# Performance work log

Measured on AMD Instinct MI355X. Metric: run time of the kernel, lower is better.

## Reference

```python
import jax, jax.numpy as jnp
import numpy as np

B, S, DIN, DOUT = 2, 2048, 4096, 11008

def setup_inputs() -> dict:
    key = jax.random.key(0)
    k1, k2, k3 = jax.random.split(key, 3)
    x = jax.random.normal(k1, (B, S, DIN), dtype=jnp.float32)
    # int8-range quantized weight codes (stored as int32 for the harness)
    w_int8 = jax.random.randint(k2, (DOUT, DIN), -127, 128, dtype=jnp.int32)
    scale = jnp.float32(0.01)
    bias = jax.random.normal(k3, (DOUT,), dtype=jnp.float32)
    return {"x": x, "w_int8": w_int8, "scale": scale, "bias": bias}

def reference(x, w_int8, scale, bias):
    # Dequantize: weight = int8_codes.astype(float32) * scale  -> [DOUT, DIN]
    weight = w_int8.astype(jnp.float32) * scale
    # F.linear: out = x @ weight.T + bias  -> [B, S, DOUT]
    out = jnp.einsum('bsi,oi->bso', x, weight) + bias
    return out
```

## Files before the change

kernel.cpp:

```cpp
#include <hip/hip_runtime.h>
#include <hip/hip_bf16.h>
#include <stdint.h>

typedef unsigned short u16;

#define M_TOT 4096
#define N_TOT 11008
#define K_TOT 4096

typedef __attribute__((ext_vector_type(4))) int i32x4;
typedef __attribute__((ext_vector_type(4))) float f32x4;
typedef __attribute__((ext_vector_type(8))) short bf16x8;

typedef const __attribute__((address_space(1))) void* gptr_t;
typedef __attribute__((address_space(3))) void* lptr_t;


__global__ __launch_bounds__(256) void quant_x(const float* __restrict__ X,
                                               uint32_t* __restrict__ Xq,
                                               float* __restrict__ scales) {
  int row = blockIdx.x;
  int t = threadIdx.x;
  const float4* xr = reinterpret_cast<const float4*>(X + (size_t)row * K_TOT) + t * 4;
  float4 v[4];
  float m = 0.f;
#pragma unroll
  for (int i = 0; i < 4; ++i) {
    v[i] = xr[i];
    m = fmaxf(m, fmaxf(fmaxf(fabsf(v[i].x), fabsf(v[i].y)),
                       fmaxf(fabsf(v[i].z), fabsf(v[i].w))));
  }
#pragma unroll
  for (int o = 1; o < 64; o <<= 1) m = fmaxf(m, __shfl_xor(m, o));
  __shared__ float wmax[4];
  int w = t >> 6, lane = t & 63;
  if (lane == 0) wmax[w] = m;
  __syncthreads();
  m = fmaxf(fmaxf(wmax[0], wmax[1]), fmaxf(wmax[2], wmax[3]));
  m = fmaxf(m, 1e-30f);
  float inv = 127.f / m;
  uint32_t q[4];
#pragma unroll
  for (int i = 0; i < 4; ++i) {
    int a = (int)rintf(v[i].x * inv), b = (int)rintf(v[i].y * inv);
    int c = (int)rintf(v[i].z * inv), d = (int)rintf(v[i].w * inv);
    q[i] = (a & 0xff) | ((b & 0xff) << 8) | ((c & 0xff) << 16) | ((uint32_t)(d & 0xff) << 24);
  }
  reinterpret_cast<uint4*>(Xq)[(size_t)row * 256 + t] = make_uint4(q[0], q[1], q[2], q[3]);
  if (t == 0) scales[row] = m / 127.f;
}

__global__ __launch_bounds__(256) void cvt_w_q(const int* __restrict__ W,
                                               uint32_t* __restrict__ Wq, int n4) {
  int i = blockIdx.x * 256 + threadIdx.x;
  int stride = gridDim.x * 256;
  for (; i < n4; i += stride) {
    int4 v = reinterpret_cast<const int4*>(W)[i];
    Wq[i] = (v.x & 0xff) | ((v.y & 0xff) << 8) | ((v.z & 0xff) << 16) |
            ((uint32_t)(v.w & 0xff) << 24);
  }
}


#define BM2 256
#define BN2 256
#define BKI 64
#define MT2 (M_TOT / BM2)
#define NT2 (N_TOT / BN2)
#define NWG2 (MT2 * NT2)
#define NKTI (K_TOT / BKI)

__global__ __launch_bounds__(512, 2) void gemm_i8_256(const int8_t* __restrict__ Xq,
                                                      const int8_t* __restrict__ Wq,
                                                      const float* __restrict__ rowsc,
                                                      const float* __restrict__ scale,
                                                      const float* __restrict__ bias,
                                                      float* __restrict__ Out) {
  __shared__ __align__(16) uint8_t lds[4][32768];

  int bid = blockIdx.x;
  int swz = (bid & 7) * (NWG2 / 8) + (bid >> 3);
  int mt = swz & (MT2 - 1);
  int nt = swz >> 4;
  int row0 = mt * BM2, col0 = nt * BN2;

  int t = threadIdx.x;
  int lane = t & 63, w = t >> 6;
  int wm = w >> 2, wn = w & 3;
  int lr = lane & 15, lk = lane >> 4;

  int ci = lane & 3;
  int rA = w * 16 + (lane >> 2);
  int cswz = ci ^ ((rA >> 1) & 3);
  size_t g0 = (size_t)(row0 + rA) * K_TOT + (size_t)(cswz * 16);
  size_t g1 = (size_t)(row0 + 128 + rA) * K_TOT + (size_t)(cswz * 16);
  size_t g2 = (size_t)(col0 + rA) * K_TOT + (size_t)(cswz * 16);
  size_t g3 = (size_t)(col0 + 128 + rA) * K_TOT + (size_t)(cswz * 16);

  auto stageA = [&](int kt) {
    size_t ko = (size_t)kt * BKI;
    char* lb = (char*)(&lds[kt & 3][0]) + w * 1024;
    __builtin_amdgcn_global_load_lds((gptr_t)(const void*)(Xq + g0 + ko), (lptr_t)(void*)(lb), 16, 0, 0);
    __builtin_amdgcn_global_load_lds((gptr_t)(const void*)(Xq + g1 + ko), (lptr_t)(void*)(lb + 8192), 16, 0, 0);
  };
  auto stageB = [&](int kt) {
    size_t ko = (size_t)kt * BKI;
    char* lb = (char*)(&lds[kt & 3][0]) + w * 1024;
    __builtin_amdgcn_global_load_lds((gptr_t)(const void*)(Wq + g2 + ko), (lptr_t)(void*)(lb + 16384), 16, 0, 0);
    __builtin_amdgcn_global_load_lds((gptr_t)(const void*)(Wq + g3 + ko), (lptr_t)(void*)(lb + 24576), 16, 0, 0);
  };

  int aoff[8], boff[4];
#pragma unroll
  for (int m = 0; m < 8; ++m) {
    int ar = wm * 128 + m * 16 + lr;
    aoff[m] = ar * BKI + ((lk ^ ((ar >> 1) & 3)) << 4);
  }
#pragma unroll
  for (int n = 0; n < 4; ++n) {
    int br = wn * 64 + n * 16 + lr;
    boff[n] = 16384 + br * BKI + ((lk ^ ((br >> 1) & 3)) << 4);
  }

  i32x4 acc[8][4] = {};

  auto compute_tile = [&](int kt) {
    const uint8_t* sb = &lds[kt & 3][0];
    i32x4 af[8], bfv[4];
#pragma unroll
    for (int m = 0; m < 8; ++m)
      af[m] = *reinterpret_cast<const i32x4*>(sb + aoff[m]);
#pragma unroll
    for (int n = 0; n < 4; ++n)
      bfv[n] = *reinterpret_cast<const i32x4*>(sb + boff[n]);
    __builtin_amdgcn_s_setprio(1);
#pragma unroll
    for (int m = 0; m < 8; ++m)
#pragma unroll
      for (int n = 0; n < 4; ++n)
        acc[m][n] = __builtin_amdgcn_mfma_i32_16x16x64_i8(af[m], bfv[n], acc[m][n], 0, 0, 0);
    __builtin_amdgcn_s_setprio(0);
  };

  stageA(0); stageB(0);
  stageA(1); stageB(1);
  stageA(2); stageB(2);
  asm volatile("s_waitcnt vmcnt(8)" ::: "memory");
  __builtin_amdgcn_s_barrier();
  asm volatile("" ::: "memory");

#pragma unroll 4
  for (int kt = 0; kt < NKTI - 3; ++kt) {
    const uint8_t* sb = &lds[kt & 3][0];
    i32x4 af[4], af2[4], bfv[4];

#pragma unroll
    for (int m = 0; m < 4; ++m)
      af[m] = *reinterpret_cast<const i32x4*>(sb + aoff[m]);
#pragma unroll
    for (int n = 0; n < 4; ++n)
      bfv[n] = *reinterpret_cast<const i32x4*>(sb + boff[n]);
#pragma unroll
    for (int m = 0; m < 4; ++m)
      af2[m] = *reinterpret_cast<const i32x4*>(sb + aoff[m + 4]);
    stageA(kt + 3);
    __builtin_amdgcn_s_barrier();
    __builtin_amdgcn_s_setprio(1);
#pragma unroll
    for (int m = 0; m < 4; ++m)
#pragma unroll
      for (int n = 0; n < 4; ++n)
        acc[m][n] = __builtin_amdgcn_mfma_i32_16x16x64_i8(af[m], bfv[n], acc[m][n], 0, 0, 0);
    __builtin_amdgcn_s_setprio(0);
    __builtin_amdgcn_s_barrier();
    asm volatile("" ::: "memory");

    stageB(kt + 3);
    asm volatile("s_waitcnt vmcnt(8)" ::: "memory");
    __builtin_amdgcn_s_barrier();
    __builtin_amdgcn_s_setprio(1);
#pragma unroll
    for (int m = 0; m < 4; ++m)
#pragma unroll
      for (int n = 0; n < 4; ++n)
        acc[m + 4][n] = __builtin_amdgcn_mfma_i32_16x16x64_i8(af2[m], bfv[n], acc[m + 4][n], 0, 0, 0);
    __builtin_amdgcn_s_setprio(0);
    __builtin_amdgcn_s_barrier();
    asm volatile("" ::: "memory");
  }

  compute_tile(NKTI - 3);
  asm volatile("s_waitcnt vmcnt(4)" ::: "memory");
  __builtin_amdgcn_s_barrier();
  asm volatile("" ::: "memory");
  compute_tile(NKTI - 2);
  asm volatile("s_waitcnt vmcnt(0)" ::: "memory");
  __builtin_amdgcn_s_barrier();
  asm volatile("" ::: "memory");
  compute_tile(NKTI - 1);

  float scl = scale[0];
  float bv[4];
#pragma unroll
  for (int n = 0; n < 4; ++n)
    bv[n] = bias[col0 + wn * 64 + n * 16 + lr];
#pragma unroll
  for (int m = 0; m < 8; ++m) {
    int rb = row0 + wm * 128 + m * 16 + lk * 4;
    f32x4 srv = *reinterpret_cast<const f32x4*>(rowsc + rb);
#pragma unroll
    for (int n = 0; n < 4; ++n) {
      int col = col0 + wn * 64 + n * 16 + lr;
#pragma unroll
      for (int r = 0; r < 4; ++r)
        Out[(size_t)(rb + r) * N_TOT + col] = (float)acc[m][n][r] * (srv[r] * scl) + bv[n];
    }
  }
}


#define BM 128
#define BN 128
#define BK 32
#define MT (M_TOT / BM)
#define NT (N_TOT / BN)
#define NWG (MT * NT)
#define NK (K_TOT / BK)

__device__ __forceinline__ unsigned pk2_rne(float lo, float hi) {
  unsigned a = __builtin_bit_cast(unsigned, lo);
  unsigned b = __builtin_bit_cast(unsigned, hi);
  a += 0x7FFFu + ((a >> 16) & 1u);
  b += 0x7FFFu + ((b >> 16) & 1u);
  return (a >> 16) | (b & 0xFFFF0000u);
}

__device__ __forceinline__ void mfma_step(const u16* sa, const u16* sb,
                                          f32x4 acc[4][4], int arow, int brow, int lk) {
  bf16x8 af[4], bfv[4];
#pragma unroll
  for (int i = 0; i < 4; ++i)
    af[i] = *reinterpret_cast<const bf16x8*>(&sa[(arow + i * 16) * BK + lk * 8]);
#pragma unroll
  for (int i = 0; i < 4; ++i)
    bfv[i] = *reinterpret_cast<const bf16x8*>(&sb[(brow + i * 16) * BK + lk * 8]);
#pragma unroll
  for (int mi = 0; mi < 4; ++mi)
#pragma unroll
    for (int ni = 0; ni < 4; ++ni)
      acc[mi][ni] = __builtin_amdgcn_mfma_f32_16x16x32_bf16(af[mi], bfv[ni], acc[mi][ni], 0, 0, 0);
}

__global__ __launch_bounds__(256, 2) void gemm_fused(const float* __restrict__ X,
                                                     const int* __restrict__ W,
                                                     const float* __restrict__ scale,
                                                     const float* __restrict__ bias,
                                                     float* __restrict__ Out) {
  __shared__ __align__(16) u16 sA[2][BM * BK];
  __shared__ __align__(16) u16 sB[2][BN * BK];

  int bid = blockIdx.x;
  int swzf = (bid & 7) * (NWG / 8) + (bid >> 3);
  int mt = swzf & (MT - 1);
  int nt = swzf >> 5;
  int row0 = mt * BM, col0 = nt * BN;

  int t = threadIdx.x;
  int lane = t & 63, w = t >> 6;
  int wm = w >> 1, wn = w & 1;
  int lr = lane & 15, lk = lane >> 4;

  int srow = t >> 3;
  int scol = (t & 7) * 4;
  const float* xg = X + (size_t)row0 * K_TOT;
  const int* wg = W + (size_t)col0 * K_TOT;

  f32x4 acc[4][4] = {};
  float4 ar[4];
  int4 br[4];

  auto load_t = [&](int kt) {
    int k0 = kt * BK;
#pragma unroll
    for (int i = 0; i < 4; ++i) {
      int r = i * 32 + srow;
      ar[i] = *reinterpret_cast<const float4*>(&xg[(size_t)r * K_TOT + k0 + scol]);
      br[i] = *reinterpret_cast<const int4*>(&wg[(size_t)r * K_TOT + k0 + scol]);
    }
  };
  auto store_t = [&](int buf) {
#pragma unroll
    for (int i = 0; i < 4; ++i) {
      int r = i * 32 + srow;
      uint2 a2, b2;
      a2.x = pk2_rne(ar[i].x, ar[i].y);
      a2.y = pk2_rne(ar[i].z, ar[i].w);
      b2.x = pk2_rne((float)br[i].x, (float)br[i].y);
      b2.y = pk2_rne((float)br[i].z, (float)br[i].w);
      *reinterpret_cast<uint2*>(&sA[buf][r * BK + scol]) = a2;
      *reinterpret_cast<uint2*>(&sB[buf][r * BK + scol]) = b2;
    }
  };

  load_t(0);
  store_t(0);
  __syncthreads();
  int cur = 0;
  for (int kt = 0; kt < NK; ++kt) {
    if (kt + 1 < NK) load_t(kt + 1);
    mfma_step(&sA[cur][0], &sB[cur][0], acc, wm * 64 + lr, wn * 64 + lr, lk);
    if (kt + 1 < NK) store_t(cur ^ 1);
    __syncthreads();
    cur ^= 1;
  }

  float scl = scale[0];
#pragma unroll
  for (int mi = 0; mi < 4; ++mi) {
    int rb = row0 + wm * 64 + mi * 16 + lk * 4;
#pragma unroll
    for (int ni = 0; ni < 4; ++ni) {
      int col = col0 + wn * 64 + ni * 16 + lr;
      float bvv = bias[col];
#pragma unroll
      for (int r = 0; r < 4; ++r)
        Out[(size_t)(rb + r) * N_TOT + col] = acc[mi][ni][r] * scl + bvv;
    }
  }
}


extern "C" void kernel_launch(void* const* d_in, const int* in_sizes, int n_in,
                              void* d_out, int out_size, void* d_ws, size_t ws_size,
                              hipStream_t stream) {
  const float* X = (const float*)d_in[0];
  const int* W = (const int*)d_in[1];
  const float* scale = (const float*)d_in[2];
  const float* bias = (const float*)d_in[3];
  float* Out = (float*)d_out;

  const size_t xq_bytes = (size_t)M_TOT * K_TOT;
  const size_t wq_bytes = (size_t)N_TOT * K_TOT;
  const size_t need = xq_bytes + wq_bytes + (size_t)M_TOT * sizeof(float);

  if (ws_size >= need) {
    int8_t* Xq = (int8_t*)d_ws;
    int8_t* Wq = Xq + xq_bytes;
    float* rowsc = (float*)(Wq + wq_bytes);
    quant_x<<<M_TOT, 256, 0, stream>>>(X, (uint32_t*)Xq, rowsc);
    cvt_w_q<<<2048, 256, 0, stream>>>(W, (uint32_t*)Wq, (int)(wq_bytes / 4));
    gemm_i8_256<<<NWG2, 512, 0, stream>>>(Xq, Wq, rowsc, scale, bias, Out);
  } else {
    gemm_fused<<<NWG, 256, 0, stream>>>(X, W, scale, bias, Out);
  }
}
```

Baseline: 253.6 us.

## Software-pipeline LDS fragment loads across K tiles with register double-buffering

```diff
diff --git a/kernel.cpp b/kernel.cpp
--- a/kernel.cpp
+++ b/kernel.cpp
@@ -124,23 +124,47 @@
 
   i32x4 acc[8][4] = {};
 
-  auto compute_tile = [&](int kt) {
-    const uint8_t* sb = &lds[kt & 3][0];
-    i32x4 af[8], bfv[4];
-#pragma unroll
-    for (int m = 0; m < 8; ++m)
-      af[m] = *reinterpret_cast<const i32x4*>(sb + aoff[m]);
-#pragma unroll
-    for (int n = 0; n < 4; ++n)
-      bfv[n] = *reinterpret_cast<const i32x4*>(sb + boff[n]);
-    __builtin_amdgcn_s_setprio(1);
-#pragma unroll
-    for (int m = 0; m < 8; ++m)
-#pragma unroll
-      for (int n = 0; n < 4; ++n)
-        acc[m][n] = __builtin_amdgcn_mfma_i32_16x16x64_i8(af[m], bfv[n], acc[m][n], 0, 0, 0);
-    __builtin_amdgcn_s_setprio(0);
-  };
+  i32x4 af[4], bfv[4];
+  i32x4 afn[4], bfn[4];
+  i32x4 af2[4];
+
+#define ALPHA(T, CA, CB, DOSTAGE, VMNSTR) do {                                   \
+    const uint8_t* sbt_ = &lds[(T) & 3][0];                                      \
+    if (DOSTAGE) stageA((T) + 3);                                                \
+    _Pragma("unroll")                                                            \
+    for (int m_ = 0; m_ < 4; ++m_)                                               \
+      af2[m_] = *reinterpret_cast<const i32x4*>(sbt_ + aoff[m_ + 4]);            \
+    __builtin_amdgcn_s_setprio(1);                                               \
+    _Pragma("unroll")                                                            \
+    for (int m_ = 0; m_ < 4; ++m_)                                               \
+      _Pragma("unroll")                                                          \
+      for (int n_ = 0; n_ < 4; ++n_)                                             \
+        acc[m_][n_] = __builtin_amdgcn_mfma_i32_16x16x64_i8(CA[m_], CB[n_], acc[m_][n_], 0, 0, 0); \
+    __builtin_amdgcn_s_setprio(0);                                               \
+    asm volatile("s_waitcnt vmcnt(" VMNSTR ")" ::: "memory");                    \
+    __builtin_amdgcn_s_barrier();                                                \
+    asm volatile("" ::: "memory");                                               \
+  } while (0)
+
+#define BETA(T, CB, NA, NB, DOSTAGE) do {                                        \
+    const uint8_t* sbn_ = &lds[((T) + 1) & 3][0];                                \
+    if (DOSTAGE) stageB((T) + 3);                                                \
+    _Pragma("unroll")                                                            \
+    for (int m_ = 0; m_ < 4; ++m_)                                               \
+      NA[m_] = *reinterpret_cast<const i32x4*>(sbn_ + aoff[m_]);                 \
+    _Pragma("unroll")                                                            \
+    for (int n_ = 0; n_ < 4; ++n_)                                               \
+      NB[n_] = *reinterpret_cast<const i32x4*>(sbn_ + boff[n_]);                 \
+    __builtin_amdgcn_s_setprio(1);                                               \
+    _Pragma("unroll")                                                            \
+    for (int m_ = 0; m_ < 4; ++m_)                                               \
+      _Pragma("unroll")                                                          \
+      for (int n_ = 0; n_ < 4; ++n_)                                             \
+        acc[m_ + 4][n_] = __builtin_amdgcn_mfma_i32_16x16x64_i8(af2[m_], CB[n_], acc[m_ + 4][n_], 0, 0, 0); \
+    __builtin_amdgcn_s_setprio(0);                                               \
+    __builtin_amdgcn_s_barrier();                                                \
+    asm volatile("" ::: "memory");                                               \
+  } while (0)
 
   stageA(0); stageB(0);
   stageA(1); stageB(1);
@@ -148,56 +172,45 @@
   asm volatile("s_waitcnt vmcnt(8)" ::: "memory");
   __builtin_amdgcn_s_barrier();
   asm volatile("" ::: "memory");
-
-#pragma unroll 4
-  for (int kt = 0; kt < NKTI - 3; ++kt) {
-    const uint8_t* sb = &lds[kt & 3][0];
-    i32x4 af[4], af2[4], bfv[4];
-
+  {
+    const uint8_t* sb0 = &lds[0][0];
+#pragma unroll
+    for (int m = 0; m < 4; ++m) af[m] = *reinterpret_cast<const i32x4*>(sb0 + aoff[m]);
+#pragma unroll
+    for (int n = 0; n < 4; ++n) bfv[n] = *reinterpret_cast<const i32x4*>(sb0 + boff[n]);
+  }
+
+#pragma unroll 2
+  for (int kt = 0; kt < 60; kt += 2) {
+    ALPHA(kt, af, bfv, true, "6");
+    BETA(kt, bfv, afn, bfn, true);
+    ALPHA(kt + 1, afn, bfn, true, "6");
+    BETA(kt + 1, bfn, af, bfv, true);
+  }
+  ALPHA(60, af, bfv, true, "6");
+  BETA(60, bfv, afn, bfn, true);
+  ALPHA(61, afn, bfn, false, "4");
+  BETA(61, bfn, af, bfv, false);
+  ALPHA(62, af, bfv, false, "0");
+  BETA(62, bfv, afn, bfn, false);
+  {
+    const uint8_t* sb3 = &lds[3][0];
+#pragma unroll
+    for (int m = 0; m < 4; ++m) af2[m] = *reinterpret_cast<const i32x4*>(sb3 + aoff[m + 4]);
 #pragma unroll
     for (int m = 0; m < 4; ++m)
-      af[m] = *reinterpret_cast<const i32x4*>(sb + aoff[m]);
-#pragma unroll
-    for (int n = 0; n < 4; ++n)
-      bfv[n] = *reinterpret_cast<const i32x4*>(sb + boff[n]);
+#pragma unroll
+      for (int n = 0; n < 4; ++n)
+        acc[m][n] = __builtin_amdgcn_mfma_i32_16x16x64_i8(afn[m], bfn[n], acc[m][n], 0, 0, 0);
 #pragma unroll
     for (int m = 0; m < 4; ++m)
-      af2[m] = *reinterpret_cast<const i32x4*>(sb + aoff[m + 4]);
-    stageA(kt + 3);
-    __builtin_amdgcn_s_barrier();
-    __builtin_amdgcn_s_setprio(1);
-#pragma unroll
-    for (int m = 0; m < 4; ++m)
 #pragma unroll
       for (int n = 0; n < 4; ++n)
-        acc[m][n] = __builtin_amdgcn_mfma_i32_16x16x64_i8(af[m], bfv[n], acc[m][n], 0, 0, 0);
-    __builtin_amdgcn_s_setprio(0);
-    __builtin_amdgcn_s_barrier();
-    asm volatile("" ::: "memory");
-
-    stageB(kt + 3);
-    asm volatile("s_waitcnt vmcnt(8)" ::: "memory");
-    __builtin_amdgcn_s_barrier();
-    __builtin_amdgcn_s_setprio(1);
-#pragma unroll
-    for (int m = 0; m < 4; ++m)
-#pragma unroll
-      for (int n = 0; n < 4; ++n)
-        acc[m + 4][n] = __builtin_amdgcn_mfma_i32_16x16x64_i8(af2[m], bfv[n], acc[m + 4][n], 0, 0, 0);
-    __builtin_amdgcn_s_setprio(0);
-    __builtin_amdgcn_s_barrier();
-    asm volatile("" ::: "memory");
-  }
-
-  compute_tile(NKTI - 3);
-  asm volatile("s_waitcnt vmcnt(4)" ::: "memory");
-  __builtin_amdgcn_s_barrier();
-  asm volatile("" ::: "memory");
-  compute_tile(NKTI - 2);
-  asm volatile("s_waitcnt vmcnt(0)" ::: "memory");
-  __builtin_amdgcn_s_barrier();
-  asm volatile("" ::: "memory");
-  compute_tile(NKTI - 1);
+        acc[m + 4][n] = __builtin_amdgcn_mfma_i32_16x16x64_i8(af2[m], bfn[n], acc[m + 4][n], 0, 0, 0);
+  }
+
+#undef ALPHA
+#undef BETA
 
   float scl = scale[0];
   float bv[4];
```

New measurement: 254.1 us. No clear change (+0.2%).
